# Optimization experiments

Hardware: AMD Instinct MI355X
Metric: run time of the kernel (lower is better)

Reference implementation:

```python
import jax, jax.numpy as jnp
import numpy as np

B, D, H, O = 4096, 1024, 8192, 1000

def _l2norm_rows(w):
    return w / jnp.maximum(jnp.linalg.norm(w, axis=1, keepdims=True), 1e-12)

def setup_inputs() -> dict:
    key = jax.random.key(0)
    k1, k2, k3 = jax.random.split(key, 3)
    x = jax.random.normal(k1, (B, D), dtype=jnp.float32)
    kohonen_weights = _l2norm_rows(jax.random.normal(k2, (H, D), dtype=jnp.float32))
    grossberg_weights = _l2norm_rows(jax.random.normal(k3, (O, H), dtype=jnp.float32))
    return {"x": x, "kohonen_weights": kohonen_weights, "grossberg_weights": grossberg_weights}

def reference(x, kohonen_weights, grossberg_weights):
    # x: [B, D] (already flat), kohonen_weights: [H, D], grossberg_weights: [O, H]
    x2 = jnp.sum(x * x, axis=1, keepdims=True)              # [B, 1]
    w2 = jnp.sum(kohonen_weights * kohonen_weights, axis=1)  # [H]
    # Euclidean cdist via the expanded quadratic form (same as torch.cdist p=2)
    sq = x2 + w2[None, :] - 2.0 * (x @ kohonen_weights.T)    # [B, H]
    distances = jnp.sqrt(jnp.maximum(sq, 0.0))
    winners = jnp.argmin(distances, axis=1)                  # [B] int
    # one_hot @ grossberg_weights.T is exactly a row gather of grossberg_weights.T
    output = jnp.take(grossberg_weights.T, winners, axis=0)  # [B, O]
    return (output, winners)
```

## Files before the change

### kernel.cpp

```cpp
#include <hip/hip_runtime.h>
#include <hip/hip_bf16.h>
#include <hip/hip_fp16.h>


#define BB 4096
#define DD 1024
#define HH 8192
#define OO 1000

#define BM 256
#define BN 128
#define BK 64
#define NTILES (HH / BN)
#define SA_TILE (BM * BK)
#define SB_TILE (BN * BK)

typedef _Float16 f16;
typedef float f32x16 __attribute__((ext_vector_type(16)));
typedef int v8i __attribute__((ext_vector_type(8)));
typedef int v4i __attribute__((ext_vector_type(4)));
union Frag { v8i v; v4i h[2]; };

typedef __attribute__((address_space(3))) uint32_t lds_u32_t;
typedef __attribute__((address_space(1))) uint32_t glb_u32_t;

__device__ __forceinline__ uint32_t packkey(float v, int col) {
  uint32_t u = __float_as_uint(v);
  uint32_t mask = (uint32_t)((int32_t)u >> 31) | 0x80000000u;
  u ^= mask;
  return (u & 0xFFFFFF80u) | (uint32_t)col;
}
__device__ __forceinline__ float unpackval(uint32_t k) {
  uint32_t u = k & 0xFFFFFF80u;
  uint32_t mask = (k & 0x80000000u) ? 0x80000000u : 0xFFFFFFFFu;
  return __uint_as_float(u ^ mask);
}
__device__ __forceinline__ void kmerge(uint32_t& k1, uint32_t& k2,
                                       uint32_t o1, uint32_t o2) {
  uint32_t mn = min(k1, o1);
  uint32_t alt = (k1 > o1) ? k2 : o2;
  k1 = max(k1, o1);
  k2 = max(mn, alt);
}

__global__ __launch_bounds__(256) void cvt_kernel(
    const float* __restrict__ x, const float* __restrict__ kw,
    uint8_t* __restrict__ xq, uint8_t* __restrict__ kq,
    const float* __restrict__ G, float* __restrict__ Gt) {
  const int tid = threadIdx.x;
  const int blk = blockIdx.x;
  __shared__ float tile[32][33];
  if (blk < (BB + HH) / 4) {
#pragma unroll
    for (int i = 0; i < 4; ++i) {
      int r = blk * 4 + i;
      const float* src = (r < BB) ? (x + (size_t)r * DD)
                                  : (kw + (size_t)(r - BB) * DD);
      uint8_t* dst = (r < BB) ? (xq + (size_t)r * DD)
                              : (kq + (size_t)(r - BB) * DD);
      float4 v = ((const float4*)src)[tid];
      int p = 0;
      p = __builtin_amdgcn_cvt_pk_fp8_f32(v.x, v.y, p, false);
      p = __builtin_amdgcn_cvt_pk_fp8_f32(v.z, v.w, p, true);
      ((int*)dst)[tid] = p;
    }
  } else {
    if (Gt == nullptr) return;
    const int tb = blk - (BB + HH) / 4;
    const int tx = tid & 31;
    const int ty = tid >> 5;
#pragma unroll 1
    for (int j4 = 0; j4 < 4; ++j4) {
      int tile_id = tb * 4 + j4;
      int h0 = (tile_id >> 5) * 32;
      int o0 = (tile_id & 31) * 32;
      __syncthreads();
#pragma unroll
      for (int j = 0; j < 4; ++j) {
        int o = o0 + ty + j * 8;
        if (o < OO) tile[ty + j * 8][tx] = G[(size_t)o * HH + h0 + tx];
      }
      __syncthreads();
#pragma unroll
      for (int j = 0; j < 4; ++j) {
        int o = o0 + tx;
        int h = h0 + ty + j * 8;
        if (o < OO) Gt[(size_t)h * OO + o] = tile[tx][ty + j * 8];
      }
    }
  }
}

__global__ __launch_bounds__(256, 2) void gemm_top2(
    const uint8_t* __restrict__ A, const uint8_t* __restrict__ Bt,
    uint4* __restrict__ pk) {
  __shared__ __align__(16) uint8_t sA[3][SA_TILE];
  __shared__ __align__(16) uint8_t sB[3][SB_TILE];
  __shared__ uint2 mk[BM][2];

  const int tid = threadIdx.x;
  const int w = tid >> 6;
  const int L = tid & 63;

  const int bid = blockIdx.y * gridDim.x + blockIdx.x;
  const int c8 = bid & 7;
  const int tt = bid >> 3;
  const int nx = c8 * 8 + (tt & 7);
  const int my = tt >> 3;
  const int m0 = my * BM;
  const int n0 = nx * BN;

  const int wr = w >> 1;
  const int wc = w & 1;

  f32x16 acc[2][4];
#pragma unroll
  for (int i = 0; i < 2; ++i)
#pragma unroll
    for (int j = 0; j < 4; ++j)
#pragma unroll
      for (int q = 0; q < 16; ++q) acc[i][j][q] = 0.f;

  const int l31 = L & 31;
  const int kh = L >> 5;

  const uint8_t* pA[4]; int dA[4];
#pragma unroll
  for (int j = 0; j < 4; ++j) {
    int c = tid + 256 * j;
    int r = c >> 2;
    int so = ((c & 3) ^ ((r >> 1) & 3)) * 16;
    pA[j] = A + (size_t)(m0 + r) * DD + so;
    dA[j] = c * 16;
  }
  const uint8_t* pB[2]; int dB[2];
#pragma unroll
  for (int j = 0; j < 2; ++j) {
    int c = tid + 256 * j;
    int r = c >> 2;
    int so = ((c & 3) ^ ((r >> 1) & 3)) * 16;
    pB[j] = Bt + (size_t)(n0 + r) * DD + so;
    dB[j] = c * 16;
  }

  auto stage = [&](int t, int p) {
#pragma unroll
    for (int j = 0; j < 4; ++j)
      __builtin_amdgcn_global_load_lds((const glb_u32_t*)(pA[j] + (size_t)t * BK),
                                       (lds_u32_t*)(&sA[p][0] + dA[j]), 16, 0, 0);
#pragma unroll
    for (int j = 0; j < 2; ++j)
      __builtin_amdgcn_global_load_lds((const glb_u32_t*)(pB[j] + (size_t)t * BK),
                                       (lds_u32_t*)(&sB[p][0] + dB[j]), 16, 0, 0);
  };

  const int t2 = (l31 >> 1) & 3;
  const int off_lo = ((2 * kh) ^ t2) * 16;
  const int off_hi = ((2 * kh + 1) ^ t2) * 16;
  const int raBase = (wr * 128 + l31) * BK;
  const int rbBase = (wc * 64 + l31) * BK;

  stage(0, 0);
  stage(1, 1);

  int cur = 0;
#pragma unroll 1
  for (int kt = 0; kt < DD / BK; ++kt) {
    if (kt == DD / BK - 1)
      asm volatile("s_waitcnt vmcnt(0) lgkmcnt(0)" ::: "memory");
    else
      asm volatile("s_waitcnt vmcnt(6) lgkmcnt(0)" ::: "memory");
    __builtin_amdgcn_s_barrier();
    asm volatile("" ::: "memory");

    if (kt < DD / BK - 2) {
      int stp = cur + 2; if (stp >= 3) stp -= 3;
      stage(kt + 2, stp);
    }

    const uint8_t* bufA = &sA[cur][0];
    const uint8_t* bufB = &sB[cur][0];

    __builtin_amdgcn_s_setprio(1);
    Frag af[4], bf[2];
#pragma unroll
    for (int j = 0; j < 4; ++j) {
      const uint8_t* base = bufA + raBase + j * 32 * BK;
      af[j].h[0] = *(const v4i*)(base + off_lo);
      af[j].h[1] = *(const v4i*)(base + off_hi);
    }
#pragma unroll
    for (int i = 0; i < 2; ++i) {
      const uint8_t* base = bufB + rbBase + i * 32 * BK;
      bf[i].h[0] = *(const v4i*)(base + off_lo);
      bf[i].h[1] = *(const v4i*)(base + off_hi);
    }
#pragma unroll
    for (int i = 0; i < 2; ++i)
#pragma unroll
      for (int j = 0; j < 4; ++j)
        acc[i][j] = __builtin_amdgcn_mfma_scale_f32_32x32x64_f8f6f4(
            bf[i].v, af[j].v, acc[i][j],
            0 , 0 ,
            0, 0x7F7F7F7Fu , 0, 0x7F7F7F7Fu);
    __builtin_amdgcn_s_setprio(0);

    cur = (cur == 2) ? 0 : cur + 1;
  }

#pragma unroll
  for (int j = 0; j < 4; ++j) {
    uint32_t k1 = 0, k2 = 0;
#pragma unroll
    for (int i = 0; i < 2; ++i) {
#pragma unroll
      for (int q = 0; q < 16; ++q) {
        int hcol = wc * 64 + i * 32 + (q & 3) + 8 * (q >> 2) + 4 * kh;
        uint32_t kj = packkey(acc[i][j][q], hcol);
        if (kj > k1) { k2 = k1; k1 = kj; }
        else k2 = max(k2, kj);
      }
    }
    uint32_t o1 = (uint32_t)__shfl_xor((int)k1, 32, 64);
    uint32_t o2 = (uint32_t)__shfl_xor((int)k2, 32, 64);
    kmerge(k1, k2, o1, o2);
    if (kh == 0) mk[wr * 128 + j * 32 + l31][wc] = make_uint2(k1, k2);
  }
  __syncthreads();
  {
    uint2 a = mk[tid][0], b = mk[tid][1];
    pk[(size_t)(m0 + tid) * NTILES + nx] = make_uint4(a.x, a.y, b.x, b.y);
  }
}

__global__ __launch_bounds__(256) void select_kernel(
    const float* __restrict__ x, const float* __restrict__ kw,
    const uint4* __restrict__ pk,
    const float* __restrict__ Gt, const float* __restrict__ G,
    float* __restrict__ out, float* __restrict__ out_w) {
  const int b = blockIdx.x * 4 + (threadIdx.x >> 6);
  const int L = threadIdx.x & 63;

  const float4* x4 = (const float4*)(x + (size_t)b * DD);
  float4 xv[4];
#pragma unroll
  for (int j = 0; j < 4; ++j) xv[j] = x4[L + 64 * j];

  uint4 kp = pk[(size_t)b * NTILES + L];

  double x2 = 0.0;
#pragma unroll
  for (int j = 0; j < 4; ++j)
    x2 += (double)xv[j].x * xv[j].x + (double)xv[j].y * xv[j].y +
          (double)xv[j].z * xv[j].z + (double)xv[j].w * xv[j].w;
#pragma unroll
  for (int msk = 1; msk < 64; msk <<= 1) x2 += __shfl_xor(x2, msk, 64);

  uint32_t m = max(kp.x, kp.z);
#pragma unroll
  for (int msk = 1; msk < 64; msk <<= 1)
    m = max(m, (uint32_t)__shfl_xor((int)m, msk, 64));
  const uint32_t thrk = packkey(unpackval(m) - 0.35f, 0);

  unsigned long long cand[4];
  cand[0] = __ballot(kp.x >= thrk);
  cand[1] = __ballot(kp.y >= thrk);
  cand[2] = __ballot(kp.z >= thrk);
  cand[3] = __ballot(kp.w >= thrk);

  double best = 1e300;
  int bestc = 0x7fffffff;
#pragma unroll 1
  for (int pass = 0; pass < 4; ++pass) {
    unsigned long long bits = cand[pass];
    uint32_t mykey = (pass == 0) ? kp.x : (pass == 1) ? kp.y
                    : (pass == 2) ? kp.z : kp.w;
    while (bits) {
      int tt = __ffsll((long long)bits) - 1;
      bits &= bits - 1;
      uint32_t kbt = (uint32_t)__shfl((int)mykey, tt, 64);
      int col = tt * 128 + (int)(kbt & 127u);
      const float4* k4 = (const float4*)(kw + (size_t)col * DD);
      double dot = 0.0, w2 = 0.0;
#pragma unroll
      for (int j = 0; j < 4; ++j) {
        float4 wv = k4[L + 64 * j];
        dot += (double)xv[j].x * wv.x + (double)xv[j].y * wv.y +
               (double)xv[j].z * wv.z + (double)xv[j].w * wv.w;
        w2 += (double)wv.x * wv.x + (double)wv.y * wv.y +
              (double)wv.z * wv.z + (double)wv.w * wv.w;
      }
#pragma unroll
      for (int msk = 1; msk < 64; msk <<= 1) {
        dot += __shfl_xor(dot, msk, 64);
        w2 += __shfl_xor(w2, msk, 64);
      }
      double sq = x2 + w2 - 2.0 * dot;
      if (sq < best || (sq == best && col < bestc)) { best = sq; bestc = col; }
    }
  }

  if (L == 0) out_w[b] = (float)bestc;
  if (Gt != nullptr) {
    const float4* gsrc = (const float4*)(Gt + (size_t)bestc * OO);
    float4* gdst = (float4*)(out + (size_t)b * OO);
#pragma unroll
    for (int j = 0; j < 4; ++j) {
      int q = L + 64 * j;
      if (q < OO / 4) gdst[q] = gsrc[q];
    }
  } else {
#pragma unroll 1
    for (int j = 0; j < 16; ++j) {
      int o = L + 64 * j;
      if (o < OO) out[(size_t)b * OO + o] = G[(size_t)o * HH + bestc];
    }
  }
}

extern "C" void kernel_launch(void* const* d_in, const int* in_sizes, int n_in,
                              void* d_out, int out_size, void* d_ws, size_t ws_size,
                              hipStream_t stream) {
  const float* x  = (const float*)d_in[0];
  const float* kw = (const float*)d_in[1];
  const float* gw = (const float*)d_in[2];
  float* out = (float*)d_out;
  float* out_w = out + (size_t)BB * OO;

  const size_t MB = 1024 * 1024;
  char* ws = (char*)d_ws;
  uint8_t* xq = (uint8_t*)(ws);
  uint8_t* kq = (uint8_t*)(ws + 4 * MB);
  uint4*   pk = (uint4*)(ws + 12 * MB);
  float*   Gt = (float*)(ws + 16 * MB);
  const size_t need = 16 * MB + sizeof(float) * (size_t)HH * OO;
  float* GtArg = (ws_size >= need) ? Gt : nullptr;

  int cvt_blocks = (BB + HH) / 4 + (GtArg ? 2048 : 0);
  cvt_kernel<<<cvt_blocks, 256, 0, stream>>>(x, kw, xq, kq, gw, GtArg);

  dim3 g(HH / BN, BB / BM);
  gemm_top2<<<g, 256, 0, stream>>>(xq, kq, pk);

  select_kernel<<<BB / 4, 256, 0, stream>>>(x, kw, pk, GtArg, gw, out, out_w);
}
```

Measured before the change: 198.9 us.

## Halve GEMM M-tile and switch to double-buffered LDS for higher occupancy

```diff
diff --git a/kernel.cpp b/kernel.cpp
--- a/kernel.cpp
+++ b/kernel.cpp
@@ -8,9 +8,10 @@
 #define HH 8192
 #define OO 1000
 
-#define BM 256
+#define BM 128
 #define BN 128
 #define BK 64
+#define NITER (DD / BK)
 #define NTILES (HH / BN)
 #define SA_TILE (BM * BK)
 #define SB_TILE (BN * BK)
@@ -91,11 +92,11 @@
   }
 }
 
-__global__ __launch_bounds__(256, 2) void gemm_top2(
+__global__ __launch_bounds__(256, 3) void gemm_top2(
     const uint8_t* __restrict__ A, const uint8_t* __restrict__ Bt,
     uint4* __restrict__ pk) {
-  __shared__ __align__(16) uint8_t sA[3][SA_TILE];
-  __shared__ __align__(16) uint8_t sB[3][SB_TILE];
+  __shared__ __align__(16) uint8_t sA[2][SA_TILE];
+  __shared__ __align__(16) uint8_t sB[2][SB_TILE];
   __shared__ uint2 mk[BM][2];
 
   const int tid = threadIdx.x;
@@ -113,39 +114,33 @@
   const int wr = w >> 1;
   const int wc = w & 1;
 
-  f32x16 acc[2][4];
+  f32x16 acc[2][2];
 #pragma unroll
   for (int i = 0; i < 2; ++i)
 #pragma unroll
-    for (int j = 0; j < 4; ++j)
+    for (int j = 0; j < 2; ++j)
 #pragma unroll
       for (int q = 0; q < 16; ++q) acc[i][j][q] = 0.f;
 
   const int l31 = L & 31;
   const int kh = L >> 5;
 
-  const uint8_t* pA[4]; int dA[4];
-#pragma unroll
-  for (int j = 0; j < 4; ++j) {
+  const uint8_t* pA[2]; int dA[2];
+  const uint8_t* pB[2]; int dB[2];
+#pragma unroll
+  for (int j = 0; j < 2; ++j) {
     int c = tid + 256 * j;
     int r = c >> 2;
     int so = ((c & 3) ^ ((r >> 1) & 3)) * 16;
     pA[j] = A + (size_t)(m0 + r) * DD + so;
+    pB[j] = Bt + (size_t)(n0 + r) * DD + so;
     dA[j] = c * 16;
-  }
-  const uint8_t* pB[2]; int dB[2];
-#pragma unroll
-  for (int j = 0; j < 2; ++j) {
-    int c = tid + 256 * j;
-    int r = c >> 2;
-    int so = ((c & 3) ^ ((r >> 1) & 3)) * 16;
-    pB[j] = Bt + (size_t)(n0 + r) * DD + so;
     dB[j] = c * 16;
   }
 
   auto stage = [&](int t, int p) {
 #pragma unroll
-    for (int j = 0; j < 4; ++j)
+    for (int j = 0; j < 2; ++j)
       __builtin_amdgcn_global_load_lds((const glb_u32_t*)(pA[j] + (size_t)t * BK),
                                        (lds_u32_t*)(&sA[p][0] + dA[j]), 16, 0, 0);
 #pragma unroll
@@ -157,34 +152,31 @@
   const int t2 = (l31 >> 1) & 3;
   const int off_lo = ((2 * kh) ^ t2) * 16;
   const int off_hi = ((2 * kh + 1) ^ t2) * 16;
-  const int raBase = (wr * 128 + l31) * BK;
+  const int raBase = (wr * 64 + l31) * BK;
   const int rbBase = (wc * 64 + l31) * BK;
 
   stage(0, 0);
-  stage(1, 1);
-
-  int cur = 0;
+
 #pragma unroll 1
-  for (int kt = 0; kt < DD / BK; ++kt) {
-    if (kt == DD / BK - 1)
-      asm volatile("s_waitcnt vmcnt(0) lgkmcnt(0)" ::: "memory");
-    else
-      asm volatile("s_waitcnt vmcnt(6) lgkmcnt(0)" ::: "memory");
+  for (int kt = 0; kt < NITER; ++kt) {
+    asm volatile("s_waitcnt lgkmcnt(0)" ::: "memory");
     __builtin_amdgcn_s_barrier();
     asm volatile("" ::: "memory");
 
-    if (kt < DD / BK - 2) {
-      int stp = cur + 2; if (stp >= 3) stp -= 3;
-      stage(kt + 2, stp);
-    }
-
-    const uint8_t* bufA = &sA[cur][0];
-    const uint8_t* bufB = &sB[cur][0];
+    if (kt < NITER - 1) {
+      stage(kt + 1, (kt + 1) & 1);
+      asm volatile("s_waitcnt vmcnt(4)" ::: "memory");
+    } else {
+      asm volatile("s_waitcnt vmcnt(0)" ::: "memory");
+    }
+
+    const uint8_t* bufA = &sA[kt & 1][0];
+    const uint8_t* bufB = &sB[kt & 1][0];
 
     __builtin_amdgcn_s_setprio(1);
-    Frag af[4], bf[2];
-#pragma unroll
-    for (int j = 0; j < 4; ++j) {
+    Frag af[2], bf[2];
+#pragma unroll
+    for (int j = 0; j < 2; ++j) {
       const uint8_t* base = bufA + raBase + j * 32 * BK;
       af[j].h[0] = *(const v4i*)(base + off_lo);
       af[j].h[1] = *(const v4i*)(base + off_hi);
@@ -198,18 +190,16 @@
 #pragma unroll
     for (int i = 0; i < 2; ++i)
 #pragma unroll
-      for (int j = 0; j < 4; ++j)
+      for (int j = 0; j < 2; ++j)
         acc[i][j] = __builtin_amdgcn_mfma_scale_f32_32x32x64_f8f6f4(
             bf[i].v, af[j].v, acc[i][j],
             0 , 0 ,
             0, 0x7F7F7F7Fu , 0, 0x7F7F7F7Fu);
     __builtin_amdgcn_s_setprio(0);
-
-    cur = (cur == 2) ? 0 : cur + 1;
-  }
-
-#pragma unroll
-  for (int j = 0; j < 4; ++j) {
+  }
+
+#pragma unroll
+  for (int j = 0; j < 2; ++j) {
     uint32_t k1 = 0, k2 = 0;
 #pragma unroll
     for (int i = 0; i < 2; ++i) {
@@ -224,10 +214,10 @@
     uint32_t o1 = (uint32_t)__shfl_xor((int)k1, 32, 64);
     uint32_t o2 = (uint32_t)__shfl_xor((int)k2, 32, 64);
     kmerge(k1, k2, o1, o2);
-    if (kh == 0) mk[wr * 128 + j * 32 + l31][wc] = make_uint2(k1, k2);
+    if (kh == 0) mk[wr * 64 + j * 32 + l31][wc] = make_uint2(k1, k2);
   }
   __syncthreads();
-  {
+  if (tid < BM) {
     uint2 a = mk[tid][0], b = mk[tid][1];
     pk[(size_t)(m0 + tid) * NTILES + nx] = make_uint4(a.x, a.y, b.x, b.y);
   }
```

After: 200.4 us. Within noise of the previous version (+0.8%).
